# Performance work log

Hardware: AMD Instinct MI355X
Metric: run time of the kernel (lower is better)

Reference implementation:

```python
import jax, jax.numpy as jnp
import numpy as np

N = 16384
D = 16          # chem_dims
K = 17          # knn k (first neighbor = self, dropped)
N_LAYERS = 3
NEG_SLOPE = 0.2
EPS = 1e-5


def group_norm(m, gamma, beta, groups=2, eps=EPS):
    # m: [N, C]; torch GroupNorm normalizes each row over each channel group
    n, c = m.shape
    g = m.reshape(n, groups, c // groups)
    mu = g.mean(-1, keepdims=True)
    var = ((g - mu) ** 2).mean(-1, keepdims=True)
    g = (g - mu) / jnp.sqrt(var + eps)
    return g.reshape(n, c) * gamma + beta


def setup_inputs() -> dict:
    key = jax.random.key(0)
    ks = jax.random.split(key, 8)
    x = jax.random.normal(ks[0], (N, 3), dtype=jnp.float32) * 10.0
    y = x  # atom-atom self graph: same point cloud
    y_atomtypes = jax.random.normal(ks[1], (N, D), dtype=jnp.float32)
    x_batch = jnp.sort(jax.random.randint(ks[2], (N,), 0, 4)).astype(jnp.int32)
    y_batch = x_batch
    Din = 2 * D + 1  # 33
    W1 = jax.random.normal(ks[3], (N_LAYERS, Din, Din), dtype=jnp.float32) * 0.1
    b1 = jnp.zeros((N_LAYERS, Din), dtype=jnp.float32)
    W2 = jax.random.normal(ks[4], (N_LAYERS, Din, D), dtype=jnp.float32) * 0.1
    b2 = jnp.zeros((N_LAYERS, D), dtype=jnp.float32)
    gamma = jnp.ones((N_LAYERS, D), dtype=jnp.float32)
    beta = jnp.zeros((N_LAYERS, D), dtype=jnp.float32)
    return {"x": x, "y": y, "y_atomtypes": y_atomtypes, "W1": W1, "b1": b1,
            "W2": W2, "b2": b2, "gamma": gamma, "beta": beta,
            "x_batch": x_batch, "y_batch": y_batch}


def knn(x, y, x_batch, y_batch, k):
    # brute-force batched KNN (keops argKmin equivalent)
    d2 = ((x * x).sum(-1)[:, None] + (y * y).sum(-1)[None, :]
          - 2.0 * x @ y.T)                                  # [N, N]
    d2 = jnp.where(x_batch[:, None] != y_batch[None, :], jnp.float32(1e30), d2)
    _, idx = jax.lax.top_k(-d2, k)                          # smallest distances
    return idx


def reference(x, y, y_atomtypes, W1, b1, W2, b2, gamma, beta, x_batch, y_batch):
    idx = knn(x, y, x_batch, y_batch, K)[:, 1:]             # drop self -> [N, K-1]
    nbr_xyz = y[idx]                                        # [N, k, 3]
    dists = ((x[:, None, :] - nbr_xyz) ** 2).sum(-1)        # [N, k]
    k = K - 1
    out = y_atomtypes
    for i in range(N_LAYERS):
        nbr = out[idx]                                      # [N, k, D] gather
        feat = jnp.concatenate(
            [jnp.broadcast_to(out[:, None, :], (out.shape[0], k, out.shape[1])),
             nbr, dists[..., None]], axis=-1)               # [N, k, 2D+1]
        h = jax.nn.leaky_relu(feat @ W1[i] + b1[i], NEG_SLOPE)
        messages = (h @ W2[i] + b2[i]).sum(1)               # sum over k -> [N, D]
        out = out + jax.nn.leaky_relu(group_norm(messages, gamma[i], beta[i]), NEG_SLOPE)
    return out
```

## Files before the change

### kernel.cpp

```cpp
#include <hip/hip_runtime.h>


#define N_PTS 16384
#define D 16
#define DIN 33
#define NEG 0.2f
#define GEPS 1e-5f
#define INFF 3.0e38f
#define INFU 0x7f800000u
#define SHRINK_AT 192

__global__ __launch_bounds__(256) void prep_kernel(const float* __restrict__ x,
                                                   float4* __restrict__ xyz4, int n) {
  int i = blockIdx.x * 256 + threadIdx.x;
  if (i < n) xyz4[i] = make_float4(x[3*i], x[3*i+1], x[3*i+2], 0.f);
}

__device__ __forceinline__ unsigned bisect16(unsigned u0, unsigned u1,
                                             unsigned u2, unsigned u3) {
  unsigned lo = 0u, hi = 0x7f800001u;
  for (int it = 0; it < 31; ++it) {
    const unsigned mid = lo + ((hi - lo) >> 1);
    const int c = __popcll(__ballot(u0 < mid)) + __popcll(__ballot(u1 < mid))
                + __popcll(__ballot(u2 < mid)) + __popcll(__ballot(u3 < mid));
    if (c >= 16) hi = mid; else lo = mid;
  }
  return lo;
}

__device__ __forceinline__ int pool_shrink(float* __restrict__ pd, int* __restrict__ pi,
                                           int pcount, float& tau, int l,
                                           unsigned long long lmask) {
  __asm__ volatile("s_waitcnt lgkmcnt(0)" ::: "memory");
  unsigned u0 = INFU, u1 = INFU, u2 = INFU, u3 = INFU;
  int j0 = 0, j1 = 0, j2 = 0, j3 = 0;
  if (l       < pcount) { u0 = __float_as_uint(pd[l]);       j0 = pi[l]; }
  if (l + 64  < pcount) { u1 = __float_as_uint(pd[l + 64]);  j1 = pi[l + 64]; }
  if (l + 128 < pcount) { u2 = __float_as_uint(pd[l + 128]); j2 = pi[l + 128]; }
  if (l + 192 < pcount) { u3 = __float_as_uint(pd[l + 192]); j3 = pi[l + 192]; }
  const unsigned t = bisect16(u0, u1, u2, u3);
  tau = __uint_as_float(t);
  int base = 0;
  { const bool k = u0 <= t; const unsigned long long m = __ballot(k);
    if (k) { const int pos = base + __popcll(m & lmask);
             pd[pos] = __uint_as_float(u0); pi[pos] = j0; }
    base += __popcll(m); }
  { const bool k = u1 <= t; const unsigned long long m = __ballot(k);
    if (k) { const int pos = base + __popcll(m & lmask);
             pd[pos] = __uint_as_float(u1); pi[pos] = j1; }
    base += __popcll(m); }
  { const bool k = u2 <= t; const unsigned long long m = __ballot(k);
    if (k) { const int pos = base + __popcll(m & lmask);
             pd[pos] = __uint_as_float(u2); pi[pos] = j2; }
    base += __popcll(m); }
  { const bool k = u3 <= t; const unsigned long long m = __ballot(k);
    if (k) { const int pos = base + __popcll(m & lmask);
             pd[pos] = __uint_as_float(u3); pi[pos] = j3; }
    base += __popcll(m); }
  return base;
}

__device__ __forceinline__ void pool_final16(const float* __restrict__ pd,
                                             const int* __restrict__ pi,
                                             int pcount, int q, int l,
                                             int* __restrict__ knn_idx,
                                             float* __restrict__ knn_d2) {
  __asm__ volatile("s_waitcnt lgkmcnt(0)" ::: "memory");
  const unsigned long long lmask = (1ull << l) - 1ull;
  unsigned u0 = INFU, u1 = INFU, u2 = INFU, u3 = INFU;
  int j0 = 0, j1 = 0, j2 = 0, j3 = 0;
  if (l       < pcount) { u0 = __float_as_uint(pd[l]);       j0 = pi[l]; }
  if (l + 64  < pcount) { u1 = __float_as_uint(pd[l + 64]);  j1 = pi[l + 64]; }
  if (l + 128 < pcount) { u2 = __float_as_uint(pd[l + 128]); j2 = pi[l + 128]; }
  if (l + 192 < pcount) { u3 = __float_as_uint(pd[l + 192]); j3 = pi[l + 192]; }
  const unsigned t = bisect16(u0, u1, u2, u3);
  int base = 0;
  { const bool k = u0 < t; const unsigned long long m = __ballot(k);
    if (k) { const int pos = base + __popcll(m & lmask);
             knn_idx[q*16+pos] = j0; knn_d2[q*16+pos] = __uint_as_float(u0); }
    base += __popcll(m); }
  { const bool k = u1 < t; const unsigned long long m = __ballot(k);
    if (k) { const int pos = base + __popcll(m & lmask);
             knn_idx[q*16+pos] = j1; knn_d2[q*16+pos] = __uint_as_float(u1); }
    base += __popcll(m); }
  { const bool k = u2 < t; const unsigned long long m = __ballot(k);
    if (k) { const int pos = base + __popcll(m & lmask);
             knn_idx[q*16+pos] = j2; knn_d2[q*16+pos] = __uint_as_float(u2); }
    base += __popcll(m); }
  { const bool k = u3 < t; const unsigned long long m = __ballot(k);
    if (k) { const int pos = base + __popcll(m & lmask);
             knn_idx[q*16+pos] = j3; knn_d2[q*16+pos] = __uint_as_float(u3); }
    base += __popcll(m); }
  const float tf = __uint_as_float(t);
  { const bool k = u0 == t; const unsigned long long m = __ballot(k);
    if (k) { const int pos = base + __popcll(m & lmask);
             if (pos < 16) { knn_idx[q*16+pos] = j0; knn_d2[q*16+pos] = tf; } }
    base += __popcll(m); }
  { const bool k = u1 == t; const unsigned long long m = __ballot(k);
    if (k) { const int pos = base + __popcll(m & lmask);
             if (pos < 16) { knn_idx[q*16+pos] = j1; knn_d2[q*16+pos] = tf; } }
    base += __popcll(m); }
  { const bool k = u2 == t; const unsigned long long m = __ballot(k);
    if (k) { const int pos = base + __popcll(m & lmask);
             if (pos < 16) { knn_idx[q*16+pos] = j2; knn_d2[q*16+pos] = tf; } }
    base += __popcll(m); }
  { const bool k = u3 == t; const unsigned long long m = __ballot(k);
    if (k) { const int pos = base + __popcll(m & lmask);
             if (pos < 16) { knn_idx[q*16+pos] = j3; knn_d2[q*16+pos] = tf; } }
    base += __popcll(m); }
}

__global__ __launch_bounds__(256) void knn_kernel(const float4* __restrict__ xyz4,
                                                  const int* __restrict__ batch,
                                                  int* __restrict__ knn_idx,
                                                  float* __restrict__ knn_d2, int n) {
  __shared__ float pd[4][256];
  __shared__ int   pi[4][256];
  const int tid = threadIdx.x;
  const int w = tid >> 6;
  const int l = tid & 63;
  const int q = blockIdx.x * 4 + w;

  const float4 Q = xyz4[q];
  const int b = batch[q];
  int lo, hi;
  { int a = 0, c = n; while (a < c) { int m = (a + c) >> 1; if (batch[m] <  b) a = m + 1; else c = m; } lo = a; }
  { int a = lo, c = n; while (a < c) { int m = (a + c) >> 1; if (batch[m] <= b) a = m + 1; else c = m; } hi = a; }

  const unsigned long long lmask = (1ull << l) - 1ull;
  float tau = INFF;
  int pcount = 0;

  int j0 = lo;
  for (; j0 + 256 <= hi; j0 += 256) {
    const int ja = j0 + l;
    const float4 P0 = xyz4[ja];
    const float4 P1 = xyz4[ja + 64];
    const float4 P2 = xyz4[ja + 128];
    const float4 P3 = xyz4[ja + 192];
    const float dx0 = Q.x-P0.x, dy0 = Q.y-P0.y, dz0 = Q.z-P0.z;
    const float dx1 = Q.x-P1.x, dy1 = Q.y-P1.y, dz1 = Q.z-P1.z;
    const float dx2 = Q.x-P2.x, dy2 = Q.y-P2.y, dz2 = Q.z-P2.z;
    const float dx3 = Q.x-P3.x, dy3 = Q.y-P3.y, dz3 = Q.z-P3.z;
    const float d20 = dx0*dx0 + dy0*dy0 + dz0*dz0;
    const float d21 = dx1*dx1 + dy1*dy1 + dz1*dz1;
    const float d22 = dx2*dx2 + dy2*dy2 + dz2*dz2;
    const float d23 = dx3*dx3 + dy3*dy3 + dz3*dz3;
    const bool p0 = (d20 < tau) && (ja        != q);
    const bool p1 = (d21 < tau) && (ja + 64   != q);
    const bool p2 = (d22 < tau) && (ja + 128  != q);
    const bool p3 = (d23 < tau) && (ja + 192  != q);
    if (__ballot(p0 | p1 | p2 | p3)) {
      { const unsigned long long m = __ballot(p0);
        if (m) { if (p0) { const int pos = pcount + __popcll(m & lmask);
                           pd[w][pos] = d20; pi[w][pos] = ja; }
                 pcount += __popcll(m);
                 if (pcount >= SHRINK_AT)
                   pcount = pool_shrink(&pd[w][0], &pi[w][0], pcount, tau, l, lmask); } }
      { const unsigned long long m = __ballot(p1);
        if (m) { if (p1) { const int pos = pcount + __popcll(m & lmask);
                           pd[w][pos] = d21; pi[w][pos] = ja + 64; }
                 pcount += __popcll(m);
                 if (pcount >= SHRINK_AT)
                   pcount = pool_shrink(&pd[w][0], &pi[w][0], pcount, tau, l, lmask); } }
      { const unsigned long long m = __ballot(p2);
        if (m) { if (p2) { const int pos = pcount + __popcll(m & lmask);
                           pd[w][pos] = d22; pi[w][pos] = ja + 128; }
                 pcount += __popcll(m);
                 if (pcount >= SHRINK_AT)
                   pcount = pool_shrink(&pd[w][0], &pi[w][0], pcount, tau, l, lmask); } }
      { const unsigned long long m = __ballot(p3);
        if (m) { if (p3) { const int pos = pcount + __popcll(m & lmask);
                           pd[w][pos] = d23; pi[w][pos] = ja + 192; }
                 pcount += __popcll(m);
                 if (pcount >= SHRINK_AT)
                   pcount = pool_shrink(&pd[w][0], &pi[w][0], pcount, tau, l, lmask); } }
    }
  }
  for (; j0 < hi; j0 += 64) {
    const int j = j0 + l;
    bool pass = false; float d2 = 0.f;
    if (j < hi) {
      const float4 P = xyz4[j];
      const float dx = Q.x - P.x, dy = Q.y - P.y, dz = Q.z - P.z;
      d2 = dx*dx + dy*dy + dz*dz;
      pass = (d2 < tau) && (j != q);
    }
    const unsigned long long m = __ballot(pass);
    if (m) {
      if (pass) {
        const int pos = pcount + __popcll(m & lmask);
        pd[w][pos] = d2; pi[w][pos] = j;
      }
      pcount += __popcll(m);
      if (pcount >= SHRINK_AT)
        pcount = pool_shrink(&pd[w][0], &pi[w][0], pcount, tau, l, lmask);
    }
  }
  pool_final16(&pd[w][0], &pi[w][0], pcount, q, l, knn_idx, knn_d2);
}

__device__ __forceinline__ void load16(const float4* __restrict__ base, int row, float* dst) {
  float4 a = base[row*4+0], b = base[row*4+1], c = base[row*4+2], d = base[row*4+3];
  dst[0]=a.x;  dst[1]=a.y;  dst[2]=a.z;  dst[3]=a.w;
  dst[4]=b.x;  dst[5]=b.y;  dst[6]=b.z;  dst[7]=b.w;
  dst[8]=c.x;  dst[9]=c.y;  dst[10]=c.z; dst[11]=c.w;
  dst[12]=d.x; dst[13]=d.y; dst[14]=d.z; dst[15]=d.w;
}

__device__ __forceinline__ float lrelu(float x) {
  return fmaxf(x, 0.f) + NEG * fminf(x, 0.f);
}

__global__ __launch_bounds__(256) void layer_kernel(
    const float* __restrict__ in, const int* __restrict__ knn_idx,
    const float* __restrict__ knn_d2,
    const float* __restrict__ W1, const float* __restrict__ b1,
    const float* __restrict__ W2, const float* __restrict__ b2,
    const float* __restrict__ gamma, const float* __restrict__ beta,
    float* __restrict__ outb) {
  __shared__ float sW1[DIN * DIN];
  __shared__ float sb1[DIN];
  __shared__ float sW2[DIN * D];
  __shared__ float sb2[D], sg[D], sbt[D];
  const int tid = threadIdx.x;
  for (int t = tid; t < DIN * DIN; t += 256) sW1[t] = W1[t];
  for (int t = tid; t < DIN * D;   t += 256) sW2[t] = W2[t];
  if (tid < DIN) sb1[tid] = b1[tid];
  if (tid < D) { sb2[tid] = b2[tid]; sg[tid] = gamma[tid]; sbt[tid] = beta[tid]; }
  __syncthreads();

  const int p = blockIdx.x * 16 + (tid >> 4);
  const int c = tid & 15;
  const float4* in4 = (const float4*)in;

  float s[16], nf[16];
  load16(in4, p, s);
  const int   nb = knn_idx[p * 16 + c];
  const float dk = knn_d2 [p * 16 + c];
  load16(in4, nb, nf);

  float h[DIN];
#pragma unroll
  for (int o = 0; o < DIN; ++o) h[o] = sb1[o] + dk * sW1[32 * DIN + o];
#pragma unroll
  for (int i = 0; i < 16; ++i) {
    const float si = s[i], ni = nf[i];
#pragma unroll
    for (int o = 0; o < DIN; ++o) {
      h[o] += si * sW1[i * DIN + o];
      h[o] += ni * sW1[(16 + i) * DIN + o];
    }
  }
#pragma unroll
  for (int o = 0; o < DIN; ++o) h[o] = lrelu(h[o]);

#pragma unroll
  for (int o = 0; o < DIN; ++o) {
    float x = h[o];
    x += __shfl_xor(x, 1);
    x += __shfl_xor(x, 2);
    x += __shfl_xor(x, 4);
    x += __shfl_xor(x, 8);
    h[o] = x;
  }

  float m = sb2[c];
#pragma unroll
  for (int i = 0; i < DIN; ++i) m += h[i] * sW2[i * D + c];

  float sum = m;
  sum += __shfl_xor(sum, 1); sum += __shfl_xor(sum, 2); sum += __shfl_xor(sum, 4);
  const float mu = sum * 0.125f;
  const float dd = m - mu;
  float sq = dd * dd;
  sq += __shfl_xor(sq, 1); sq += __shfl_xor(sq, 2); sq += __shfl_xor(sq, 4);
  const float var = sq * 0.125f;
  float yv = dd * (1.0f / sqrtf(var + GEPS));
  yv = yv * sg[c] + sbt[c];

  const float selfc = in[p * 16 + c];
  outb[p * 16 + c] = selfc + lrelu(yv);
}

extern "C" void kernel_launch(void* const* d_in, const int* in_sizes, int n_in,
                              void* d_out, int out_size, void* d_ws, size_t ws_size,
                              hipStream_t stream) {
  const float* x     = (const float*)d_in[0];
  const float* yat   = (const float*)d_in[2];
  const float* W1    = (const float*)d_in[3];
  const float* b1    = (const float*)d_in[4];
  const float* W2    = (const float*)d_in[5];
  const float* b2    = (const float*)d_in[6];
  const float* gamma = (const float*)d_in[7];
  const float* beta  = (const float*)d_in[8];
  const int*   xb    = (const int*)d_in[9];
  float* out = (float*)d_out;

  char* ws = (char*)d_ws;
  float4* xyz4 = (float4*)(ws);
  int*    kidx = (int*)  (ws + 262144);
  float*  kd2  = (float*)(ws + 262144 + 1048576);
  float*  bufA = (float*)(ws + 262144 + 2*1048576);
  float*  bufB = (float*)(ws + 262144 + 3*1048576);

  prep_kernel<<<N_PTS / 256, 256, 0, stream>>>(x, xyz4, N_PTS);
  knn_kernel<<<N_PTS / 4, 256, 0, stream>>>(xyz4, xb, kidx, kd2, N_PTS);
  layer_kernel<<<N_PTS / 16, 256, 0, stream>>>(yat,  kidx, kd2,
      W1 + 0*DIN*DIN, b1 + 0*DIN, W2 + 0*DIN*D, b2 + 0*D, gamma + 0*D, beta + 0*D, bufA);
  layer_kernel<<<N_PTS / 16, 256, 0, stream>>>(bufA, kidx, kd2,
      W1 + 1*DIN*DIN, b1 + 1*DIN, W2 + 1*DIN*D, b2 + 1*D, gamma + 1*D, beta + 1*D, bufB);
  layer_kernel<<<N_PTS / 16, 256, 0, stream>>>(bufB, kidx, kd2,
      W1 + 2*DIN*DIN, b1 + 2*DIN, W2 + 2*DIN*D, b2 + 2*D, gamma + 2*D, beta + 2*D, out);
}
```

Before: 223.4 us.

## Hoist self-feature W1 projection out of per-neighbor loop via shared memory

The self-feature half of the first MLP layer (s @ W1[:16] + b1) is identical for all 16 neighbors of a point. It is now computed once per point, split across the 16 lanes with each lane producing two outputs, and shared through a small LDS buffer. This removes about half of the per-neighbor FMAs. W1 is also no longer staged into shared memory; neighbor-half weights are read directly from global (uniform, likely scalar or cached loads). The code relies on an s_waitcnt instead of a __syncthreads, which is only safe because the 16 lanes of a group sit in the same wavefront.

```diff
diff --git a/kernel.cpp b/kernel.cpp
--- a/kernel.cpp
+++ b/kernel.cpp
@@ -219,38 +219,51 @@
     const float* __restrict__ W2, const float* __restrict__ b2,
     const float* __restrict__ gamma, const float* __restrict__ beta,
     float* __restrict__ outb) {
-  __shared__ float sW1[DIN * DIN];
-  __shared__ float sb1[DIN];
   __shared__ float sW2[DIN * D];
   __shared__ float sb2[D], sg[D], sbt[D];
+  __shared__ float sU[16][36];
   const int tid = threadIdx.x;
-  for (int t = tid; t < DIN * DIN; t += 256) sW1[t] = W1[t];
-  for (int t = tid; t < DIN * D;   t += 256) sW2[t] = W2[t];
-  if (tid < DIN) sb1[tid] = b1[tid];
+  for (int t = tid; t < DIN * D; t += 256) sW2[t] = W2[t];
   if (tid < D) { sb2[tid] = b2[tid]; sg[tid] = gamma[tid]; sbt[tid] = beta[tid]; }
   __syncthreads();
 
-  const int p = blockIdx.x * 16 + (tid >> 4);
+  const int g = tid >> 4;
   const int c = tid & 15;
+  const int p = blockIdx.x * 16 + g;
   const float4* in4 = (const float4*)in;
 
-  float s[16], nf[16];
+  float s[16];
   load16(in4, p, s);
+
+  float ua = b1[c], ub = b1[16 + c];
+#pragma unroll
+  for (int i = 0; i < 16; ++i) {
+    ua += s[i] * W1[i * DIN + c];
+    ub += s[i] * W1[i * DIN + 16 + c];
+  }
+  sU[g][c] = ua;
+  sU[g][16 + c] = ub;
+  if (c == 15) {
+    float uz = b1[32];
+#pragma unroll
+    for (int i = 0; i < 16; ++i) uz += s[i] * W1[i * DIN + 32];
+    sU[g][32] = uz;
+  }
+  __asm__ volatile("s_waitcnt lgkmcnt(0)" ::: "memory");
+
   const int   nb = knn_idx[p * 16 + c];
   const float dk = knn_d2 [p * 16 + c];
+  float nf[16];
   load16(in4, nb, nf);
 
   float h[DIN];
 #pragma unroll
-  for (int o = 0; o < DIN; ++o) h[o] = sb1[o] + dk * sW1[32 * DIN + o];
+  for (int o = 0; o < DIN; ++o) h[o] = sU[g][o] + dk * W1[32 * DIN + o];
 #pragma unroll
   for (int i = 0; i < 16; ++i) {
-    const float si = s[i], ni = nf[i];
-#pragma unroll
-    for (int o = 0; o < DIN; ++o) {
-      h[o] += si * sW1[i * DIN + o];
-      h[o] += ni * sW1[(16 + i) * DIN + o];
-    }
+    const float ni = nf[i];
+#pragma unroll
+    for (int o = 0; o < DIN; ++o) h[o] += ni * W1[(16 + i) * DIN + o];
   }
 #pragma unroll
   for (int o = 0; o < DIN; ++o) h[o] = lrelu(h[o]);
```

Result: faster. 205.7 us (-7.9%).
